# Optimization experiments

Hardware: AMD Instinct MI355X
Metric: run time of the kernel (lower is better)

## Reference

```python
import jax, jax.numpy as jnp
import numpy as np

B, S, D_IN, H, D_HEAD = 8, 1024, 768, 12, 64

def setup_inputs() -> dict:
    key = jax.random.key(0)
    k1, k2, k3, k4 = jax.random.split(key, 4)
    x = jax.random.normal(k1, (B, S, D_IN), dtype=jnp.float32)
    # per-head projection weights, stacked: [H, d_in, d_head]
    scale = 1.0 / np.sqrt(D_IN)
    Wq = jax.random.normal(k2, (H, D_IN, D_HEAD), dtype=jnp.float32) * scale
    Wk = jax.random.normal(k3, (H, D_IN, D_HEAD), dtype=jnp.float32) * scale
    Wv = jax.random.normal(k4, (H, D_IN, D_HEAD), dtype=jnp.float32) * scale
    return {"x": x, "Wq": Wq, "Wk": Wk, "Wv": Wv}

def reference(x, Wq, Wk, Wv) -> jnp.ndarray:
    # Batched equivalent of the Python loop over heads + concat.
    q = jnp.einsum('bsd,hde->bhse', x, Wq)  # [B,H,S,Dh]
    k = jnp.einsum('bsd,hde->bhse', x, Wk)
    v = jnp.einsum('bsd,hde->bhse', x, Wv)
    scores = jnp.einsum('bhse,bhte->bhst', q, k) / jnp.sqrt(jnp.asarray(D_HEAD, x.dtype))
    causal = jnp.tril(jnp.ones((S, S), dtype=bool))  # [S,S]
    scores = jnp.where(causal, scores, jnp.asarray(-jnp.inf, x.dtype))
    attn = jax.nn.softmax(scores, axis=-1)  # dropout p=0.0 -> identity
    ctx = jnp.einsum('bhst,bhte->bhse', attn, v)  # [B,H,S,Dh]
    # concat heads along last dim -> [B,S,H*Dh]
    return jnp.transpose(ctx, (0, 2, 1, 3)).reshape(B, S, H * D_HEAD)
```

## Files before the change

### kernel.cpp

```cpp
#include <hip/hip_runtime.h>

typedef short short8 __attribute__((ext_vector_type(8)));
typedef float f32x4 __attribute__((ext_vector_type(4)));
typedef float f32x16 __attribute__((ext_vector_type(16)));

#define SQ   1024
#define DIN  768
#define NH   12
#define DH   64
#define SCL2 0.1803368801111243f

static __device__ __forceinline__ ushort f2bf(float f) {
  union { float f; unsigned u; } v; v.f = f;
  unsigned u = v.u;
  unsigned r = (u + 0x7FFFu + ((u >> 16) & 1u)) >> 16;
  return (ushort)r;
}
static __device__ __forceinline__ unsigned cvtpk(float a, float b) {
  unsigned r;
  asm("v_cvt_pk_bf16_f32 %0, %1, %2" : "=v"(r) : "v"(a), "v"(b));
  return r;
}

static __device__ __forceinline__ void gload_lds16(const ushort* g, ushort* l) {
  __builtin_amdgcn_global_load_lds(
      (const __attribute__((address_space(1))) unsigned*)(g),
      (__attribute__((address_space(3))) unsigned*)(l),
      16, 0, 0);
}

__global__ __launch_bounds__(256) void k_convert_x(const float* __restrict__ x,
                                                   ushort* __restrict__ xb) {
  int i = (blockIdx.x * 256 + threadIdx.x) * 8;
  float4 v0 = *reinterpret_cast<const float4*>(x + i);
  float4 v1 = *reinterpret_cast<const float4*>(x + i + 4);
  uint4 o;
  o.x = cvtpk(v0.x, v0.y); o.y = cvtpk(v0.z, v0.w);
  o.z = cvtpk(v1.x, v1.y); o.w = cvtpk(v1.z, v1.w);
  *reinterpret_cast<uint4*>(xb + i) = o;
}

__global__ __launch_bounds__(256) void k_prep_w(const float* __restrict__ Wq,
                                                const float* __restrict__ Wk,
                                                const float* __restrict__ Wv,
                                                ushort* __restrict__ wt) {
  __shared__ ushort tile[64][65];
  const int mh = blockIdx.x;
  const int m = mh / 12, h = mh % 12;
  const int d0 = blockIdx.y * 64;
  const float* W = (m == 0 ? Wq : (m == 1 ? Wk : Wv)) + h * DIN * DH;
  ushort* outp = wt + (size_t)mh * DH * DIN;
  #pragma unroll
  for (int p = 0; p < 16; ++p) {
    int idx = p * 256 + threadIdx.x;
    int d = idx >> 6, e = idx & 63;
    tile[d][e] = f2bf(W[(d0 + d) * DH + e]);
  }
  __syncthreads();
  #pragma unroll
  for (int p = 0; p < 16; ++p) {
    int idx = p * 256 + threadIdx.x;
    int e = idx >> 6, d = idx & 63;
    outp[e * DIN + d0 + d] = tile[d][e];
  }
}

__global__ __launch_bounds__(256) void k_proj(const ushort* __restrict__ xb,
                                              const ushort* __restrict__ wt,
                                              ushort* __restrict__ qo,
                                              ushort* __restrict__ ko,
                                              ushort* __restrict__ vto) {
  __shared__ __align__(16) ushort Sb[24576];

  const int brow = blockIdx.x * 128;
  const int bn   = blockIdx.y * 128;
  const int w    = threadIdx.x >> 6, lane = threadIdx.x & 63;
  const int ql   = lane & 31, hi = lane >> 5;
  const int wm   = w >> 1, wn = w & 1;

  const int srow  = threadIdx.x >> 2;
  const int sslot = (threadIdx.x & 3) ^ (srow & 3) ^ ((srow >> 2) & 3);
  const ushort* gA = xb + (size_t)(brow + srow) * DIN + sslot * 8;
  const ushort* gB = wt + (size_t)(bn   + srow) * DIN + sslot * 8;

  f32x16 acc[2][2];
  #pragma unroll
  for (int i = 0; i < 2; ++i)
    #pragma unroll
    for (int j = 0; j < 2; ++j)
      #pragma unroll
      for (int r = 0; r < 16; ++r) acc[i][j][r] = 0.f;

  const int frq = (ql & 3) ^ ((ql >> 2) & 3);

#define STAGEP(bi, tt) do {                                               \
    const int k0_ = (tt) * 32;                                            \
    ushort* la_ = Sb + (bi) * 4096 + threadIdx.x * 8;                     \
    ushort* lb_ = Sb + 12288 + (bi) * 4096 + threadIdx.x * 8;             \
    gload_lds16(gA + k0_,            la_);                                \
    gload_lds16(gA + k0_ + 64 * DIN, la_ + 2048);                         \
    gload_lds16(gB + k0_,            lb_);                                \
    gload_lds16(gB + k0_ + 64 * DIN, lb_ + 2048);                         \
  } while (0)

  STAGEP(0, 0);
  STAGEP(1, 1);

  int cur = 0;
  #pragma unroll 1
  for (int t = 0; t < 24; ++t) {
    if (t < 23) asm volatile("s_waitcnt vmcnt(4)" ::: "memory");
    else        asm volatile("s_waitcnt vmcnt(0)" ::: "memory");
    __builtin_amdgcn_sched_barrier(0);
    __builtin_amdgcn_s_barrier();
    __builtin_amdgcn_sched_barrier(0);
    if (t + 2 < 24) {
      int nb = cur + 2; if (nb >= 3) nb -= 3;
      STAGEP(nb, t + 2);
    }
    short8 a[2][2], b[2][2];
    #pragma unroll
    for (int ai = 0; ai < 2; ++ai) {
      const int row = wm * 64 + ai * 32 + ql;
      #pragma unroll
      for (int ks = 0; ks < 2; ++ks)
        a[ai][ks] = *reinterpret_cast<const short8*>(
            &Sb[cur * 4096 + row * 32 + (((ks * 2 + hi) ^ frq) * 8)]);
    }
    #pragma unroll
    for (int ci = 0; ci < 2; ++ci) {
      const int row = wn * 64 + ci * 32 + ql;
      #pragma unroll
      for (int ks = 0; ks < 2; ++ks)
        b[ci][ks] = *reinterpret_cast<const short8*>(
            &Sb[12288 + cur * 4096 + row * 32 + (((ks * 2 + hi) ^ frq) * 8)]);
    }
    #pragma unroll
    for (int ai = 0; ai < 2; ++ai)
      #pragma unroll
      for (int ci = 0; ci < 2; ++ci) {
        acc[ai][ci] = __builtin_amdgcn_mfma_f32_32x32x16_bf16(a[ai][0], b[ci][0], acc[ai][ci], 0, 0, 0);
        acc[ai][ci] = __builtin_amdgcn_mfma_f32_32x32x16_bf16(a[ai][1], b[ci][1], acc[ai][ci], 0, 0, 0);
      }
    cur += 1; if (cur >= 3) cur = 0;
  }
#undef STAGEP

  __syncthreads();

  ushort* ldsw = Sb + w * 4096;
  const int mh = blockIdx.y * 2 + wn;
  const int m = mh / 12, h = mh % 12;
  const int c = lane & 7;

  if (m < 2) {
    #pragma unroll
    for (int ai = 0; ai < 2; ++ai)
      #pragma unroll
      for (int ci = 0; ci < 2; ++ci)
        #pragma unroll
        for (int r = 0; r < 16; ++r) {
          int sl = ai * 32 + (r & 3) + 8 * (r >> 2) + 4 * hi;
          int e  = ci * 32 + ql;
          ldsw[sl * 64 + (e ^ ((sl & 7) << 3))] = f2bf(acc[ai][ci][r]);
        }
    asm volatile("s_waitcnt lgkmcnt(0)" ::: "memory");
    ushort* dst = (m == 0) ? qo : ko;
    #pragma unroll
    for (int it = 0; it < 8; ++it) {
      int sl = it * 8 + (lane >> 3);
      short8 vv = *reinterpret_cast<const short8*>(&ldsw[sl * 64 + ((c * 8) ^ ((sl & 7) << 3))]);
      int rg = brow + wm * 64 + sl;
      int b_ = rg >> 10, s_ = rg & 1023;
      *reinterpret_cast<short8*>(dst + ((size_t)(b_ * 12 + h) * SQ + s_) * DH + c * 8) = vv;
    }
  } else {
    #pragma unroll
    for (int ai = 0; ai < 2; ++ai)
      #pragma unroll
      for (int ci = 0; ci < 2; ++ci)
        #pragma unroll
        for (int r = 0; r < 16; ++r) {
          int sl = ai * 32 + (r & 3) + 8 * (r >> 2) + 4 * hi;
          int e  = ci * 32 + ql;
          ldsw[e * 64 + (sl ^ ((e & 7) << 3))] = f2bf(acc[ai][ci][r]);
        }
    asm volatile("s_waitcnt lgkmcnt(0)" ::: "memory");
    #pragma unroll
    for (int it = 0; it < 8; ++it) {
      int e = it * 8 + (lane >> 3);
      short8 vv = *reinterpret_cast<const short8*>(&ldsw[e * 64 + ((c * 8) ^ ((e & 7) << 3))]);
      int rg = brow + wm * 64 + c * 8;
      int b_ = rg >> 10, s_ = rg & 1023;
      *reinterpret_cast<short8*>(vto + ((size_t)(b_ * 12 + h) * DH + e) * SQ + s_) = vv;
    }
  }
}

__global__ __launch_bounds__(256, 3) void k_attn(const ushort* __restrict__ qi,
                                                 const ushort* __restrict__ ki,
                                                 const ushort* __restrict__ vti,
                                                 float* __restrict__ out) {
  __shared__ __align__(16) ushort Kb[2][64 * 64];
  __shared__ __align__(16) ushort Vb[2][64 * 64];

  const int f = blockIdx.x;
  const int g = f >> 8, r_ = f & 255;
  const int qt = ((r_ & 7) + g * 3) & 7;
  const int bh = g * 32 + (r_ >> 3);
  const int b = bh / 12, h = bh % 12;
  const int w = threadIdx.x >> 6, lane = threadIdx.x & 63;
  const int ql = lane & 31, hi = lane >> 5;
  const int q0 = qt * 128 + w * 32;
  const int nt = (q0 >> 6) + 1;
  const int ntmax = 2 * qt + 2;
  const ushort* qb = qi  + (size_t)bh * SQ * DH;
  const ushort* kb = ki  + (size_t)bh * SQ * DH;
  const ushort* vb = vti + (size_t)bh * DH * SQ;

  short8 qf[4];
  #pragma unroll
  for (int m = 0; m < 4; ++m)
    qf[m] = *reinterpret_cast<const short8*>(qb + (size_t)(q0 + ql) * DH + m * 16 + hi * 8);

  f32x16 o0, o1;
  #pragma unroll
  for (int r = 0; r < 16; ++r) { o0[r] = 0.f; o1[r] = 0.f; }
  float m_run = -1e30f, l_run = 0.f;

#define STAGE(bufi, tt) do {                                                                   \
    const int kv0_ = (tt) * 64;                                                                \
    const int t0 = threadIdx.x, t1 = threadIdx.x + 256;                                        \
    gload_lds16(kb + (size_t)(kv0_ + (t0 >> 3)) * DH + (((t0 & 7) ^ ((t0 >> 3) & 7)) * 8),     \
                &Kb[bufi][0] + t0 * 8);                                                        \
    gload_lds16(kb + (size_t)(kv0_ + (t1 >> 3)) * DH + (((t1 & 7) ^ ((t1 >> 3) & 7)) * 8),     \
                &Kb[bufi][0] + t1 * 8);                                                        \
    gload_lds16(vb + (size_t)(t0 >> 3) * SQ + kv0_ + (((t0 & 7) ^ ((t0 >> 3) & 7)) * 8),       \
                &Vb[bufi][0] + t0 * 8);                                                        \
    gload_lds16(vb + (size_t)(t1 >> 3) * SQ + kv0_ + (((t1 & 7) ^ ((t1 >> 3) & 7)) * 8),       \
                &Vb[bufi][0] + t1 * 8);                                                        \
  } while (0)

  STAGE(0, 0);
  __syncthreads();

  int cur = 0;
  #pragma unroll 1
  for (int t = 0; t < ntmax; ++t) {
    if (t + 1 < ntmax) STAGE(cur ^ 1, t + 1);

    if (t < nt) {
      const int kv0 = t * 64;
      const ushort* Kc = &Kb[cur][0];
      const ushort* Vc = &Vb[cur][0];

      f32x16 s0, s1;
      #pragma unroll
      for (int r = 0; r < 16; ++r) { s0[r] = 0.f; s1[r] = 0.f; }
      #pragma unroll
      for (int m = 0; m < 4; ++m) {
        short8 kf = *reinterpret_cast<const short8*>(Kc + ql * 64 + ((2 * m + hi) ^ (ql & 7)) * 8);
        s0 = __builtin_amdgcn_mfma_f32_32x32x16_bf16(kf, qf[m], s0, 0, 0, 0);
      }
      #pragma unroll
      for (int m = 0; m < 4; ++m) {
        short8 kf = *reinterpret_cast<const short8*>(Kc + (32 + ql) * 64 + ((2 * m + hi) ^ (ql & 7)) * 8);
        s1 = __builtin_amdgcn_mfma_f32_32x32x16_bf16(kf, qf[m], s1, 0, 0, 0);
      }

      if (t == nt - 1) {
        const int qg = q0 + ql;
        #pragma unroll
        for (int r = 0; r < 16; ++r) {
          int kvl = (r & 3) + 8 * (r >> 2) + 4 * hi;
          if (kv0 + kvl      > qg) s0[r] = -1e30f;
          if (kv0 + 32 + kvl > qg) s1[r] = -1e30f;
        }
      }

      float tr[16];
      #pragma unroll
      for (int r = 0; r < 16; ++r) tr[r] = fmaxf(s0[r], s1[r]);
      #pragma unroll
      for (int off = 8; off >= 1; off >>= 1)
        #pragma unroll
        for (int i = 0; i < 8; ++i)
          if (i < off) tr[i] = fmaxf(tr[i], tr[i + off]);
      float mt = fmaxf(tr[0], __shfl_xor(tr[0], 32));

      if (__any(mt > m_run + 40.0f)) {
        float mnew = fmaxf(m_run, mt);
        float corr = exp2f((m_run - mnew) * SCL2);
        l_run *= corr; m_run = mnew;
        #pragma unroll
        for (int r = 0; r < 16; ++r) {
          float cr = __shfl(corr, (r & 3) + 8 * (r >> 2) + 4 * hi);
          o0[r] *= cr; o1[r] *= cr;
        }
      }
      #pragma unroll
      for (int r = 0; r < 16; ++r) {
        s0[r] = exp2f((s0[r] - m_run) * SCL2);
        s1[r] = exp2f((s1[r] - m_run) * SCL2);
      }
      #pragma unroll
      for (int r = 0; r < 16; ++r) tr[r] = s0[r] + s1[r];
      #pragma unroll
      for (int off = 8; off >= 1; off >>= 1)
        #pragma unroll
        for (int i = 0; i < 8; ++i)
          if (i < off) tr[i] = tr[i] + tr[i + off];
      l_run += tr[0] + __shfl_xor(tr[0], 32);

#define PV_CHUNK(SV, CC, KC) do {                                                              \
        unsigned wa = cvtpk(SV[(CC) * 8 + 0], SV[(CC) * 8 + 1]);                               \
        unsigned wb = cvtpk(SV[(CC) * 8 + 2], SV[(CC) * 8 + 3]);                               \
        unsigned wc = cvtpk(SV[(CC) * 8 + 4], SV[(CC) * 8 + 5]);                               \
        unsigned wd = cvtpk(SV[(CC) * 8 + 6], SV[(CC) * 8 + 7]);                               \
        unsigned xa = __shfl_xor(wa, 32), xb2 = __shfl_xor(wb, 32);                            \
        unsigned xc = __shfl_xor(wc, 32), xd = __shfl_xor(wd, 32);                             \
        uint4 pw;                                                                              \
        pw.x = hi ? xc : wa;  pw.y = hi ? xd : wb;                                             \
        pw.z = hi ? wc : xa;  pw.w = hi ? wd : xb2;                                            \
        short8 pa = *reinterpret_cast<short8*>(&pw);                                           \
        short8 vf0 = *reinterpret_cast<const short8*>(Vc + ql * 64 +                           \
                       ((2 * (KC) + hi) ^ (ql & 7)) * 8);                                      \
        o0 = __builtin_amdgcn_mfma_f32_32x32x16_bf16(pa, vf0, o0, 0, 0, 0);                    \
        short8 vf1 = *reinterpret_cast<const short8*>(Vc + (32 + ql) * 64 +                    \
                       ((2 * (KC) + hi) ^ (ql & 7)) * 8);                                      \
        o1 = __builtin_amdgcn_mfma_f32_32x32x16_bf16(pa, vf1, o1, 0, 0, 0);                    \
      } while (0)

      PV_CHUNK(s0, 0, 0);
      PV_CHUNK(s0, 1, 1);
      PV_CHUNK(s1, 0, 2);
      PV_CHUNK(s1, 1, 3);
#undef PV_CHUNK
    }

    __syncthreads();
    cur ^= 1;
  }
#undef STAGE

  float rl = 1.0f / l_run;
  #pragma unroll
  for (int r = 0; r < 16; ++r) {
    int base = (r & 3) + 8 * (r >> 2) + 4 * hi;
    float sc_ = __shfl(rl, base);
    int qg = q0 + base;
    float* op = out + ((size_t)b * SQ + qg) * (NH * DH) + h * DH;
    op[ql]      = o0[r] * sc_;
    op[32 + ql] = o1[r] * sc_;
  }
}

extern "C" void kernel_launch(void* const* d_in, const int* in_sizes, int n_in,
                              void* d_out, int out_size, void* d_ws, size_t ws_size,
                              hipStream_t stream) {
  const float* x  = (const float*)d_in[0];
  const float* Wq = (const float*)d_in[1];
  const float* Wk = (const float*)d_in[2];
  const float* Wv = (const float*)d_in[3];
  float* out = (float*)d_out;

  char* ws = (char*)d_ws;
  ushort* xb = (ushort*)(ws);
  ushort* wt = (ushort*)(ws + 12582912);
  ushort* q  = (ushort*)(ws + 16121856);
  ushort* k  = (ushort*)(ws + 28704768);
  ushort* vt = (ushort*)(ws + 41287680);

  k_convert_x<<<3072, 256, 0, stream>>>(x, xb);
  k_prep_w<<<dim3(36, 12), 256, 0, stream>>>(Wq, Wk, Wv, wt);
  k_proj<<<dim3(64, 18), 256, 0, stream>>>(xb, wt, q, k, vt);
  k_attn<<<768, 256, 0, stream>>>(q, k, vt, out);
}
```

Before: 172.2 us.

## Merge prep kernels and enlarge projection GEMM tile to 256x128

Folds the x-conversion and weight-transpose kernels into one launch, with block ranges picking the role, which removes one kernel launch and its drain. The projection GEMM tile grows from 128 to 256 rows per block, so each wave computes 4x2 MFMA tiles and each weight tile loaded into LDS is reused twice as often. The grid is halved to 576 blocks with larger LDS use and more accumulator registers. This risks lower occupancy and a worse wave count across the CUs.

```diff
diff --git a/kernel.cpp b/kernel.cpp
--- a/kernel.cpp
+++ b/kernel.cpp
@@ -29,50 +29,52 @@
       16, 0, 0);
 }
 
-__global__ __launch_bounds__(256) void k_convert_x(const float* __restrict__ x,
-                                                   ushort* __restrict__ xb) {
-  int i = (blockIdx.x * 256 + threadIdx.x) * 8;
-  float4 v0 = *reinterpret_cast<const float4*>(x + i);
-  float4 v1 = *reinterpret_cast<const float4*>(x + i + 4);
-  uint4 o;
-  o.x = cvtpk(v0.x, v0.y); o.y = cvtpk(v0.z, v0.w);
-  o.z = cvtpk(v1.x, v1.y); o.w = cvtpk(v1.z, v1.w);
-  *reinterpret_cast<uint4*>(xb + i) = o;
-}
-
-__global__ __launch_bounds__(256) void k_prep_w(const float* __restrict__ Wq,
-                                                const float* __restrict__ Wk,
-                                                const float* __restrict__ Wv,
-                                                ushort* __restrict__ wt) {
+__global__ __launch_bounds__(256) void k_prep(const float* __restrict__ x,
+                                              const float* __restrict__ Wq,
+                                              const float* __restrict__ Wk,
+                                              const float* __restrict__ Wv,
+                                              ushort* __restrict__ xb,
+                                              ushort* __restrict__ wt) {
   __shared__ ushort tile[64][65];
-  const int mh = blockIdx.x;
-  const int m = mh / 12, h = mh % 12;
-  const int d0 = blockIdx.y * 64;
-  const float* W = (m == 0 ? Wq : (m == 1 ? Wk : Wv)) + h * DIN * DH;
-  ushort* outp = wt + (size_t)mh * DH * DIN;
-  #pragma unroll
-  for (int p = 0; p < 16; ++p) {
-    int idx = p * 256 + threadIdx.x;
-    int d = idx >> 6, e = idx & 63;
-    tile[d][e] = f2bf(W[(d0 + d) * DH + e]);
-  }
-  __syncthreads();
-  #pragma unroll
-  for (int p = 0; p < 16; ++p) {
-    int idx = p * 256 + threadIdx.x;
-    int e = idx >> 6, d = idx & 63;
-    outp[e * DIN + d0 + d] = tile[d][e];
-  }
-}
-
-__global__ __launch_bounds__(256) void k_proj(const ushort* __restrict__ xb,
-                                              const ushort* __restrict__ wt,
-                                              ushort* __restrict__ qo,
-                                              ushort* __restrict__ ko,
-                                              ushort* __restrict__ vto) {
-  __shared__ __align__(16) ushort Sb[24576];
-
-  const int brow = blockIdx.x * 128;
+  if (blockIdx.x < 3072) {
+    int i = (blockIdx.x * 256 + threadIdx.x) * 8;
+    float4 v0 = *reinterpret_cast<const float4*>(x + i);
+    float4 v1 = *reinterpret_cast<const float4*>(x + i + 4);
+    uint4 o;
+    o.x = cvtpk(v0.x, v0.y); o.y = cvtpk(v0.z, v0.w);
+    o.z = cvtpk(v1.x, v1.y); o.w = cvtpk(v1.z, v1.w);
+    *reinterpret_cast<uint4*>(xb + i) = o;
+  } else {
+    const int idx = blockIdx.x - 3072;
+    const int mh = idx % 36;
+    const int m = mh / 12, h = mh % 12;
+    const int d0 = (idx / 36) * 64;
+    const float* W = (m == 0 ? Wq : (m == 1 ? Wk : Wv)) + h * DIN * DH;
+    ushort* outp = wt + (size_t)mh * DH * DIN;
+    #pragma unroll
+    for (int p = 0; p < 16; ++p) {
+      int ii = p * 256 + threadIdx.x;
+      int d = ii >> 6, e = ii & 63;
+      tile[d][e] = f2bf(W[(d0 + d) * DH + e]);
+    }
+    __syncthreads();
+    #pragma unroll
+    for (int p = 0; p < 16; ++p) {
+      int ii = p * 256 + threadIdx.x;
+      int e = ii >> 6, d = ii & 63;
+      outp[e * DIN + d0 + d] = tile[d][e];
+    }
+  }
+}
+
+__global__ __launch_bounds__(256, 2) void k_proj(const ushort* __restrict__ xb,
+                                                 const ushort* __restrict__ wt,
+                                                 ushort* __restrict__ qo,
+                                                 ushort* __restrict__ ko,
+                                                 ushort* __restrict__ vto) {
+  __shared__ __align__(16) ushort Sb[36864];
+
+  const int brow = blockIdx.x * 256;
   const int bn   = blockIdx.y * 128;
   const int w    = threadIdx.x >> 6, lane = threadIdx.x & 63;
   const int ql   = lane & 31, hi = lane >> 5;
@@ -83,9 +85,9 @@
   const ushort* gA = xb + (size_t)(brow + srow) * DIN + sslot * 8;
   const ushort* gB = wt + (size_t)(bn   + srow) * DIN + sslot * 8;
 
-  f32x16 acc[2][2];
-  #pragma unroll
-  for (int i = 0; i < 2; ++i)
+  f32x16 acc[4][2];
+  #pragma unroll
+  for (int i = 0; i < 4; ++i)
     #pragma unroll
     for (int j = 0; j < 2; ++j)
       #pragma unroll
@@ -95,12 +97,14 @@
 
 #define STAGEP(bi, tt) do {                                               \
     const int k0_ = (tt) * 32;                                            \
-    ushort* la_ = Sb + (bi) * 4096 + threadIdx.x * 8;                     \
-    ushort* lb_ = Sb + 12288 + (bi) * 4096 + threadIdx.x * 8;             \
-    gload_lds16(gA + k0_,            la_);                                \
-    gload_lds16(gA + k0_ + 64 * DIN, la_ + 2048);                         \
-    gload_lds16(gB + k0_,            lb_);                                \
-    gload_lds16(gB + k0_ + 64 * DIN, lb_ + 2048);                         \
+    ushort* la_ = Sb + (bi) * 8192 + threadIdx.x * 8;                     \
+    ushort* lb_ = Sb + 24576 + (bi) * 4096 + threadIdx.x * 8;             \
+    gload_lds16(gA + k0_,             la_);                               \
+    gload_lds16(gA + k0_ +  64 * DIN, la_ + 2048);                        \
+    gload_lds16(gA + k0_ + 128 * DIN, la_ + 4096);                        \
+    gload_lds16(gA + k0_ + 192 * DIN, la_ + 6144);                        \
+    gload_lds16(gB + k0_,             lb_);                               \
+    gload_lds16(gB + k0_ +  64 * DIN, lb_ + 2048);                        \
   } while (0)
 
   STAGEP(0, 0);
@@ -109,7 +113,7 @@
   int cur = 0;
   #pragma unroll 1
   for (int t = 0; t < 24; ++t) {
-    if (t < 23) asm volatile("s_waitcnt vmcnt(4)" ::: "memory");
+    if (t < 23) asm volatile("s_waitcnt vmcnt(6)" ::: "memory");
     else        asm volatile("s_waitcnt vmcnt(0)" ::: "memory");
     __builtin_amdgcn_sched_barrier(0);
     __builtin_amdgcn_s_barrier();
@@ -118,14 +122,14 @@
       int nb = cur + 2; if (nb >= 3) nb -= 3;
       STAGEP(nb, t + 2);
     }
-    short8 a[2][2], b[2][2];
-    #pragma unroll
-    for (int ai = 0; ai < 2; ++ai) {
-      const int row = wm * 64 + ai * 32 + ql;
+    short8 a[4][2], b[2][2];
+    #pragma unroll
+    for (int ai = 0; ai < 4; ++ai) {
+      const int row = wm * 128 + ai * 32 + ql;
       #pragma unroll
       for (int ks = 0; ks < 2; ++ks)
         a[ai][ks] = *reinterpret_cast<const short8*>(
-            &Sb[cur * 4096 + row * 32 + (((ks * 2 + hi) ^ frq) * 8)]);
+            &Sb[cur * 8192 + row * 32 + (((ks * 2 + hi) ^ frq) * 8)]);
     }
     #pragma unroll
     for (int ci = 0; ci < 2; ++ci) {
@@ -133,10 +137,10 @@
       #pragma unroll
       for (int ks = 0; ks < 2; ++ks)
         b[ci][ks] = *reinterpret_cast<const short8*>(
-            &Sb[12288 + cur * 4096 + row * 32 + (((ks * 2 + hi) ^ frq) * 8)]);
-    }
-    #pragma unroll
-    for (int ai = 0; ai < 2; ++ai)
+            &Sb[24576 + cur * 4096 + row * 32 + (((ks * 2 + hi) ^ frq) * 8)]);
+    }
+    #pragma unroll
+    for (int ai = 0; ai < 4; ++ai)
       #pragma unroll
       for (int ci = 0; ci < 2; ++ci) {
         acc[ai][ci] = __builtin_amdgcn_mfma_f32_32x32x16_bf16(a[ai][0], b[ci][0], acc[ai][ci], 0, 0, 0);
@@ -153,46 +157,49 @@
   const int m = mh / 12, h = mh % 12;
   const int c = lane & 7;
 
-  if (m < 2) {
-    #pragma unroll
-    for (int ai = 0; ai < 2; ++ai)
-      #pragma unroll
-      for (int ci = 0; ci < 2; ++ci)
-        #pragma unroll
-        for (int r = 0; r < 16; ++r) {
-          int sl = ai * 32 + (r & 3) + 8 * (r >> 2) + 4 * hi;
-          int e  = ci * 32 + ql;
-          ldsw[sl * 64 + (e ^ ((sl & 7) << 3))] = f2bf(acc[ai][ci][r]);
-        }
-    asm volatile("s_waitcnt lgkmcnt(0)" ::: "memory");
-    ushort* dst = (m == 0) ? qo : ko;
-    #pragma unroll
-    for (int it = 0; it < 8; ++it) {
-      int sl = it * 8 + (lane >> 3);
-      short8 vv = *reinterpret_cast<const short8*>(&ldsw[sl * 64 + ((c * 8) ^ ((sl & 7) << 3))]);
-      int rg = brow + wm * 64 + sl;
-      int b_ = rg >> 10, s_ = rg & 1023;
-      *reinterpret_cast<short8*>(dst + ((size_t)(b_ * 12 + h) * SQ + s_) * DH + c * 8) = vv;
-    }
-  } else {
-    #pragma unroll
-    for (int ai = 0; ai < 2; ++ai)
-      #pragma unroll
-      for (int ci = 0; ci < 2; ++ci)
-        #pragma unroll
-        for (int r = 0; r < 16; ++r) {
-          int sl = ai * 32 + (r & 3) + 8 * (r >> 2) + 4 * hi;
-          int e  = ci * 32 + ql;
-          ldsw[e * 64 + (sl ^ ((e & 7) << 3))] = f2bf(acc[ai][ci][r]);
-        }
-    asm volatile("s_waitcnt lgkmcnt(0)" ::: "memory");
-    #pragma unroll
-    for (int it = 0; it < 8; ++it) {
-      int e = it * 8 + (lane >> 3);
-      short8 vv = *reinterpret_cast<const short8*>(&ldsw[e * 64 + ((c * 8) ^ ((e & 7) << 3))]);
-      int rg = brow + wm * 64 + c * 8;
-      int b_ = rg >> 10, s_ = rg & 1023;
-      *reinterpret_cast<short8*>(vto + ((size_t)(b_ * 12 + h) * DH + e) * SQ + s_) = vv;
+  #pragma unroll
+  for (int p = 0; p < 2; ++p) {
+    if (m < 2) {
+      #pragma unroll
+      for (int a2 = 0; a2 < 2; ++a2)
+        #pragma unroll
+        for (int ci = 0; ci < 2; ++ci)
+          #pragma unroll
+          for (int r = 0; r < 16; ++r) {
+            int sl = a2 * 32 + (r & 3) + 8 * (r >> 2) + 4 * hi;
+            int e  = ci * 32 + ql;
+            ldsw[sl * 64 + (e ^ ((sl & 7) << 3))] = f2bf(acc[p * 2 + a2][ci][r]);
+          }
+      asm volatile("s_waitcnt lgkmcnt(0)" ::: "memory");
+      ushort* dst = (m == 0) ? qo : ko;
+      #pragma unroll
+      for (int it = 0; it < 8; ++it) {
+        int sl = it * 8 + (lane >> 3);
+        short8 vv = *reinterpret_cast<const short8*>(&ldsw[sl * 64 + ((c * 8) ^ ((sl & 7) << 3))]);
+        int rg = brow + wm * 128 + p * 64 + sl;
+        int b_ = rg >> 10, s_ = rg & 1023;
+        *reinterpret_cast<short8*>(dst + ((size_t)(b_ * 12 + h) * SQ + s_) * DH + c * 8) = vv;
+      }
+    } else {
+      #pragma unroll
+      for (int a2 = 0; a2 < 2; ++a2)
+        #pragma unroll
+        for (int ci = 0; ci < 2; ++ci)
+          #pragma unroll
+          for (int r = 0; r < 16; ++r) {
+            int sl = a2 * 32 + (r & 3) + 8 * (r >> 2) + 4 * hi;
+            int e  = ci * 32 + ql;
+            ldsw[e * 64 + (sl ^ ((e & 7) << 3))] = f2bf(acc[p * 2 + a2][ci][r]);
+          }
+      asm volatile("s_waitcnt lgkmcnt(0)" ::: "memory");
+      #pragma unroll
+      for (int it = 0; it < 8; ++it) {
+        int e = it * 8 + (lane >> 3);
+        short8 vv = *reinterpret_cast<const short8*>(&ldsw[e * 64 + ((c * 8) ^ ((e & 7) << 3))]);
+        int rg = brow + wm * 128 + p * 64 + c * 8;
+        int b_ = rg >> 10, s_ = rg & 1023;
+        *reinterpret_cast<short8*>(vto + ((size_t)(b_ * 12 + h) * DH + e) * SQ + s_) = vv;
+      }
     }
   }
 }
@@ -371,8 +378,7 @@
   ushort* k  = (ushort*)(ws + 28704768);
   ushort* vt = (ushort*)(ws + 41287680);
 
-  k_convert_x<<<3072, 256, 0, stream>>>(x, xb);
-  k_prep_w<<<dim3(36, 12), 256, 0, stream>>>(Wq, Wk, Wv, wt);
-  k_proj<<<dim3(64, 18), 256, 0, stream>>>(xb, wt, q, k, vt);
+  k_prep<<<3504, 256, 0, stream>>>(x, Wq, Wk, Wv, xb, wt);
+  k_proj<<<dim3(32, 18), 256, 0, stream>>>(xb, wt, q, k, vt);
   k_attn<<<768, 256, 0, stream>>>(q, k, vt, out);
 }
```

Measured after the change: 182.0 us. 1.06x slower.
